# Optimization experiments

Hardware: AMD Instinct MI355X
Metric: run time of the kernel (lower is better)

The kernel has to match this reference:

```python
import jax, jax.numpy as jnp
import numpy as np


def setup_inputs() -> dict:
    key = jax.random.key(0)
    ks = jax.random.split(key, 8)
    B, C, H, W = 4, 512, 64, 64
    M = C // 8
    sq = 1.0 / np.sqrt(C)
    return {
        "x": jax.random.normal(ks[0], (B, C, H, W), jnp.float32),
        "Wq": jax.random.normal(ks[1], (M, C), jnp.float32) * sq,
        "bq": jnp.zeros((M,), jnp.float32),
        "Wk": jax.random.normal(ks[2], (M, C), jnp.float32) * sq,
        "bk": jnp.zeros((M,), jnp.float32),
        "Wv": jax.random.normal(ks[3], (C, C), jnp.float32) * sq,
        "bv": jnp.zeros((C,), jnp.float32),
        "gamma": jax.random.uniform(ks[4], (1,), jnp.float32),
    }


def reference(x, Wq, bq, Wk, bk, Wv, bv, gamma):
    B, C, H, W = x.shape
    N = H * W
    xf = x.reshape(B, C, N)  # flatten spatial -> [B, C, N]
    # 1x1 convs are channel-mixing matmuls
    q = jnp.einsum('mc,bcn->bmn', Wq, xf) + bq[None, :, None]  # [B, M, N]
    k = jnp.einsum('mc,bcn->bmn', Wk, xf) + bk[None, :, None]  # [B, M, N]
    v = jnp.einsum('dc,bcn->bdn', Wv, xf) + bv[None, :, None]  # [B, C, N]
    # sim[b,i,j] = <q[:, i], k[:, j]>, softmax over j
    sim = jnp.einsum('bmi,bmj->bij', q, k)  # [B, N, N]
    attn = jax.nn.softmax(sim, axis=-1)
    # feat[b,c,i] = sum_j v[b,c,j] * attn[b,i,j]
    feat = jnp.einsum('bcj,bij->bci', v, attn)  # [B, C, N]
    out = gamma[0] * feat.reshape(B, C, H, W) + x
    return out
```

## Files before the change

kernel.cpp:

```cpp
#include <hip/hip_runtime.h>

typedef _Float16 f16;
typedef _Float16 f16x8 __attribute__((ext_vector_type(8)));
typedef float    f32x4 __attribute__((ext_vector_type(4)));
typedef unsigned int u32x2 __attribute__((ext_vector_type(2)));

#define B_ 4
#define C_ 512
#define N_ 4096
#define M_ 64

__device__ __forceinline__ unsigned pk2(float a, float b) {
    union { f16 h[2]; unsigned u; } t;
    t.h[0] = (f16)a; t.h[1] = (f16)b;
    return t.u;
}

__global__ __launch_bounds__(256) void transpose_cast(
    const float* __restrict__ x, f16* __restrict__ xtf)
{
    __shared__ float sT[64][65];
    const int n0 = blockIdx.x * 64;
    const int c0 = blockIdx.y * 64;
    const int b  = blockIdx.z;
    const int tid = threadIdx.x;

    #pragma unroll
    for (int i = 0; i < 4; ++i) {
        int e = i * 256 + tid;
        int c = e >> 4;
        int n4 = (e & 15) * 4;
        float4 v = *(const float4*)(x + ((size_t)(b * C_ + c0 + c)) * N_ + n0 + n4);
        sT[c][n4 + 0] = v.x; sT[c][n4 + 1] = v.y;
        sT[c][n4 + 2] = v.z; sT[c][n4 + 3] = v.w;
    }
    __syncthreads();

    const int w = tid >> 6, lane = tid & 63, l15 = lane & 15, quad = lane >> 4;
    #pragma unroll
    for (int j = 0; j < 2; ++j) {
        const int fb  = w * 2 + j;
        const int lnt = fb >> 1, lck = fb & 1;
        const int nl  = lnt * 16 + l15;
        const int cb  = lck * 32 + quad * 8;
        f16x8 o;
        #pragma unroll
        for (int jj = 0; jj < 8; ++jj) o[jj] = (f16)sT[cb + jj][nl];
        const int ntg = (n0 >> 4) + lnt;
        const int ck  = (c0 >> 5) + lck;
        size_t idx = (((size_t)(b * 256 + ntg)) * 16 + ck) * 512 + lane * 8;
        *(f16x8*)(xtf + idx) = o;
    }
}

__global__ __launch_bounds__(512) void qkv_gemm(
    const f16* __restrict__ xtf,
    const float* __restrict__ Wq, const float* __restrict__ bq,
    const float* __restrict__ Wk, const float* __restrict__ bk,
    const float* __restrict__ Wv, const float* __restrict__ bv,
    f16* __restrict__ qt, f16* __restrict__ ktf, f16* __restrict__ vf)
{
    const int tid  = threadIdx.x;
    const int w    = tid >> 6;
    const int lane = tid & 63;
    const int l15  = lane & 15;
    const int quad = lane >> 4;
    const int nBase = blockIdx.x * 128;
    const int oseg  = blockIdx.y;
    const int b     = blockIdx.z;
    const int ot16  = w & 3;
    const int nhalf = w >> 2;

    const float* Wsel;
    if (oseg == 0)      Wsel = Wq;
    else if (oseg == 1) Wsel = Wk;
    else                Wsel = Wv + (size_t)(oseg - 2) * 64 * C_;

    const int orow = ot16 * 16 + l15;
    const float* wp = Wsel + (size_t)orow * C_ + quad * 8;

    const f16* xfb[4];
    #pragma unroll
    for (int ns = 0; ns < 4; ++ns) {
        int ntg = (nBase >> 4) + nhalf * 4 + ns;
        xfb[ns] = xtf + (((size_t)(b * 256 + ntg)) * 16) * 512 + lane * 8;
    }

    f32x4 acc[4] = {};

    float4 w0c = *(const float4*)(wp);
    float4 w1c = *(const float4*)(wp + 4);
    f16x8 b8c[4];
    #pragma unroll
    for (int ns = 0; ns < 4; ++ns) b8c[ns] = *(const f16x8*)(xfb[ns]);

    for (int ck = 0; ck < 16; ++ck) {
        float4 w0n, w1n;
        f16x8  b8n[4];
        if (ck + 1 < 16) {
            w0n = *(const float4*)(wp + ck * 32 + 32);
            w1n = *(const float4*)(wp + ck * 32 + 36);
            #pragma unroll
            for (int ns = 0; ns < 4; ++ns)
                b8n[ns] = *(const f16x8*)(xfb[ns] + (ck + 1) * 512);
        }
        f16x8 a8;
        a8[0]=(f16)w0c.x; a8[1]=(f16)w0c.y; a8[2]=(f16)w0c.z; a8[3]=(f16)w0c.w;
        a8[4]=(f16)w1c.x; a8[5]=(f16)w1c.y; a8[6]=(f16)w1c.z; a8[7]=(f16)w1c.w;
        #pragma unroll
        for (int ns = 0; ns < 4; ++ns)
            acc[ns] = __builtin_amdgcn_mfma_f32_16x16x32_f16(a8, b8c[ns], acc[ns], 0, 0, 0);
        w0c = w0n; w1c = w1n;
        #pragma unroll
        for (int ns = 0; ns < 4; ++ns) b8c[ns] = b8n[ns];
    }

    #pragma unroll
    for (int ns = 0; ns < 4; ++ns) {
        int n = nBase + nhalf * 64 + ns * 16 + l15;
        #pragma unroll
        for (int r = 0; r < 4; ++r) {
            int olocal = ot16 * 16 + quad * 4 + r;
            float bias;
            if (oseg == 0)      bias = bq[olocal];
            else if (oseg == 1) bias = bk[olocal];
            else                bias = bv[(oseg - 2) * 64 + olocal];
            f16 h = (f16)(acc[ns][r] + bias);
            if (oseg == 0) {
                qt[((size_t)(b * N_ + n)) * M_ + olocal] = h;
            } else if (oseg == 1) {
                size_t idx = (((size_t)b * 256 + (n >> 4)) * 2 + (olocal >> 5)) * 512
                           + (size_t)((((olocal >> 3) & 3) * 16 + (n & 15)) * 8) + (olocal & 7);
                ktf[idx] = h;
            } else {
                int c = (oseg - 2) * 64 + olocal;
                size_t idx = ((size_t)b * (C_ * N_)) + (size_t)(c >> 4) * 65536
                           + (size_t)(n >> 6) * 1024 + (size_t)((n >> 5) & 1) * 512
                           + (size_t)((((n >> 3) & 3) * 16 + (c & 15)) * 8) + (n & 7);
                vf[idx] = h;
            }
        }
    }
}

__global__ __launch_bounds__(512, 2) void attn(
    const f16* __restrict__ qt, const f16* __restrict__ ktf,
    const f16* __restrict__ vf, const float* __restrict__ x,
    const float* __restrict__ gamma, float* __restrict__ out)
{
    __shared__ __align__(16) char Pb[2][8192];
    __shared__ float mxs[8][4][16];
    __shared__ float lss[8][4][16];

    const int tid  = threadIdx.x;
    const int w    = tid >> 6;
    const int lane = tid & 63;
    const int l15  = lane & 15;
    const int quad = lane >> 4;
    const int jt   = w & 3;
    const int ish  = w >> 2;
    const int is0  = ish * 2, is1 = is0 + 1;

    const int lin  = blockIdx.x;
    const int b    = (lin & 7) >> 1;
    const int iblk = ((lin >> 3) << 1) | (lin & 1);
    const int i0   = iblk * 64;

    const f16* kln = ktf + (size_t)b * (N_ * M_) + lane * 8;
    const f16* vln = vf  + (size_t)b * (C_ * N_) + lane * 8;

    f16x8 bqf[4][2];
    #pragma unroll
    for (int is = 0; is < 4; ++is)
        #pragma unroll
        for (int kh = 0; kh < 2; ++kh)
            bqf[is][kh] = *(const f16x8*)(qt + ((size_t)(b * N_ + i0 + is * 16 + l15)) * M_
                                          + kh * 32 + quad * 8);

    float mx[4];
    #pragma unroll
    for (int is = 0; is < 4; ++is) mx[is] = -3.0e38f;
    {
        const f16* kw = kln + (size_t)(w * 512) * 64;
        f16x8 akc[4][2];
        #pragma unroll
        for (int t = 0; t < 4; ++t)
            #pragma unroll
            for (int kh = 0; kh < 2; ++kh)
                akc[t][kh] = *(const f16x8*)(kw + t * 1024 + kh * 512);

        #pragma unroll 2
        for (int jj = 0; jj < 512; jj += 64) {
            f16x8 akn[4][2];
            if (jj + 64 < 512) {
                const f16* kn = kw + (size_t)(jj + 64) * 64;
                #pragma unroll
                for (int t = 0; t < 4; ++t)
                    #pragma unroll
                    for (int kh = 0; kh < 2; ++kh)
                        akn[t][kh] = *(const f16x8*)(kn + t * 1024 + kh * 512);
            }
            #pragma unroll
            for (int t = 0; t < 4; ++t) {
                #pragma unroll
                for (int is = 0; is < 4; ++is) {
                    f32x4 s = {};
                    s = __builtin_amdgcn_mfma_f32_16x16x32_f16(akc[t][0], bqf[is][0], s, 0, 0, 0);
                    s = __builtin_amdgcn_mfma_f32_16x16x32_f16(akc[t][1], bqf[is][1], s, 0, 0, 0);
                    mx[is] = fmaxf(mx[is], fmaxf(fmaxf(s[0], s[1]), fmaxf(s[2], s[3])));
                }
            }
            #pragma unroll
            for (int t = 0; t < 4; ++t)
                #pragma unroll
                for (int kh = 0; kh < 2; ++kh)
                    akc[t][kh] = akn[t][kh];
        }
    }
    #pragma unroll
    for (int is = 0; is < 4; ++is) {
        mx[is] = fmaxf(mx[is], __shfl_xor(mx[is], 16, 64));
        mx[is] = fmaxf(mx[is], __shfl_xor(mx[is], 32, 64));
    }
    if (lane < 16) {
        #pragma unroll
        for (int is = 0; is < 4; ++is) mxs[w][is][lane] = mx[is];
    }
    __syncthreads();
    float m0 = -3.0e38f, m1 = -3.0e38f;
    #pragma unroll
    for (int w2 = 0; w2 < 8; ++w2) {
        m0 = fmaxf(m0, mxs[w2][is0][l15]);
        m1 = fmaxf(m1, mxs[w2][is1][l15]);
    }

    f32x4 acc[4][4] = {};
    float lp0 = 0.f, lp1 = 0.f;

    char* pbB = (char*)&Pb[0][0];
    const int swz = (l15 & 7) << 4;
    const int wb0 = ((is0 * 16 + l15) * 128 + (jt * 16 + quad * 4) * 2) ^ swz;
    const int wb1 = wb0 + 2048;
    int rb[4][2];
    #pragma unroll
    for (int is = 0; is < 4; ++is)
        #pragma unroll
        for (int kh = 0; kh < 2; ++kh)
            rb[is][kh] = ((is * 16 + l15) * 128 + kh * 64 + quad * 16) ^ swz;

    const f16* kp = kln + (size_t)(jt * 16) * 64;
    const int cw = w * 4;

    f16x8 ak0 = *(const f16x8*)(kp);
    f16x8 ak1 = *(const f16x8*)(kp + 512);
    {
        f32x4 s0 = {}, s1 = {};
        s0 = __builtin_amdgcn_mfma_f32_16x16x32_f16(ak0, bqf[is0][0], s0, 0, 0, 0);
        s0 = __builtin_amdgcn_mfma_f32_16x16x32_f16(ak1, bqf[is0][1], s0, 0, 0, 0);
        s1 = __builtin_amdgcn_mfma_f32_16x16x32_f16(ak0, bqf[is1][0], s1, 0, 0, 0);
        s1 = __builtin_amdgcn_mfma_f32_16x16x32_f16(ak1, bqf[is1][1], s1, 0, 0, 0);
        float p0 = __expf(s0[0] - m0), p1 = __expf(s0[1] - m0);
        float p2 = __expf(s0[2] - m0), p3 = __expf(s0[3] - m0);
        lp0 += (p0 + p1) + (p2 + p3);
        u32x2 pw0 = { pk2(p0, p1), pk2(p2, p3) };
        *(u32x2*)(pbB + wb0) = pw0;
        float q0 = __expf(s1[0] - m1), q1 = __expf(s1[1] - m1);
        float q2 = __expf(s1[2] - m1), q3 = __expf(s1[3] - m1);
        lp1 += (q0 + q1) + (q2 + q3);
        u32x2 pw1 = { pk2(q0, q1), pk2(q2, q3) };
        *(u32x2*)(pbB + wb1) = pw1;
    }
    ak0 = *(const f16x8*)(kp + 4096);
    ak1 = *(const f16x8*)(kp + 4096 + 512);
    f16x8 vc0[4], vc1[4];
    #pragma unroll
    for (int ct = 0; ct < 4; ++ct) {
        vc0[ct] = *(const f16x8*)(vln + (size_t)(cw + ct) * 65536);
        vc1[ct] = *(const f16x8*)(vln + (size_t)(cw + ct) * 65536 + 512);
    }
    __syncthreads();

    #pragma unroll 2
    for (int t = 0; t < 63; ++t) {
        const int cb = (t & 1) * 8192;
        const int nb = ((t + 1) & 1) * 8192;

        f16x8 pbf[4][2];
        #pragma unroll
        for (int is = 0; is < 4; ++is)
            #pragma unroll
            for (int kh = 0; kh < 2; ++kh)
                pbf[is][kh] = *(const f16x8*)(pbB + cb + rb[is][kh]);

        f32x4 s0 = {}, s1 = {};
        s0 = __builtin_amdgcn_mfma_f32_16x16x32_f16(ak0, bqf[is0][0], s0, 0, 0, 0);
        s0 = __builtin_amdgcn_mfma_f32_16x16x32_f16(ak1, bqf[is0][1], s0, 0, 0, 0);
        s1 = __builtin_amdgcn_mfma_f32_16x16x32_f16(ak0, bqf[is1][0], s1, 0, 0, 0);
        s1 = __builtin_amdgcn_mfma_f32_16x16x32_f16(ak1, bqf[is1][1], s1, 0, 0, 0);

        if (t + 2 < 64) {
            ak0 = *(const f16x8*)(kp + (size_t)(t + 2) * 4096);
            ak1 = *(const f16x8*)(kp + (size_t)(t + 2) * 4096 + 512);
        }
        const f16* vt = vln + (size_t)(t + 1) * 1024;
        f16x8 vn0[4], vn1[4];
        #pragma unroll
        for (int ct = 0; ct < 4; ++ct) {
            vn0[ct] = *(const f16x8*)(vt + (size_t)(cw + ct) * 65536);
            vn1[ct] = *(const f16x8*)(vt + (size_t)(cw + ct) * 65536 + 512);
        }

        {
            float p0 = __expf(s0[0] - m0), p1 = __expf(s0[1] - m0);
            float p2 = __expf(s0[2] - m0), p3 = __expf(s0[3] - m0);
            lp0 += (p0 + p1) + (p2 + p3);
            u32x2 pw = { pk2(p0, p1), pk2(p2, p3) };
            *(u32x2*)(pbB + nb + wb0) = pw;
        }
        {
            float q0 = __expf(s1[0] - m1), q1 = __expf(s1[1] - m1);
            float q2 = __expf(s1[2] - m1), q3 = __expf(s1[3] - m1);
            lp1 += (q0 + q1) + (q2 + q3);
            u32x2 pw = { pk2(q0, q1), pk2(q2, q3) };
            *(u32x2*)(pbB + nb + wb1) = pw;
        }

        __builtin_amdgcn_s_setprio(1);
        #pragma unroll
        for (int ct = 0; ct < 4; ++ct)
            #pragma unroll
            for (int is = 0; is < 4; ++is)
                acc[ct][is] = __builtin_amdgcn_mfma_f32_16x16x32_f16(vc0[ct], pbf[is][0], acc[ct][is], 0, 0, 0);
        #pragma unroll
        for (int ct = 0; ct < 4; ++ct)
            #pragma unroll
            for (int is = 0; is < 4; ++is)
                acc[ct][is] = __builtin_amdgcn_mfma_f32_16x16x32_f16(vc1[ct], pbf[is][1], acc[ct][is], 0, 0, 0);
        __builtin_amdgcn_s_setprio(0);

        __syncthreads();

        #pragma unroll
        for (int ct = 0; ct < 4; ++ct) { vc0[ct] = vn0[ct]; vc1[ct] = vn1[ct]; }
    }

    {
        const int cb = (63 & 1) * 8192;
        f16x8 pbf[4][2];
        #pragma unroll
        for (int is = 0; is < 4; ++is)
            #pragma unroll
            for (int kh = 0; kh < 2; ++kh)
                pbf[is][kh] = *(const f16x8*)(pbB + cb + rb[is][kh]);
        #pragma unroll
        for (int ct = 0; ct < 4; ++ct)
            #pragma unroll
            for (int is = 0; is < 4; ++is)
                acc[ct][is] = __builtin_amdgcn_mfma_f32_16x16x32_f16(vc0[ct], pbf[is][0], acc[ct][is], 0, 0, 0);
        #pragma unroll
        for (int ct = 0; ct < 4; ++ct)
            #pragma unroll
            for (int is = 0; is < 4; ++is)
                acc[ct][is] = __builtin_amdgcn_mfma_f32_16x16x32_f16(vc1[ct], pbf[is][1], acc[ct][is], 0, 0, 0);
    }

    lp0 += __shfl_xor(lp0, 16, 64);
    lp0 += __shfl_xor(lp0, 32, 64);
    lp1 += __shfl_xor(lp1, 16, 64);
    lp1 += __shfl_xor(lp1, 32, 64);
    if (lane < 16) { lss[w][is0][lane] = lp0; lss[w][is1][lane] = lp1; }
    __syncthreads();

    float linv[4];
    #pragma unroll
    for (int is = 0; is < 4; ++is) {
        const int wb = (is >> 1) * 4;
        float l = (lss[wb + 0][is][l15] + lss[wb + 1][is][l15])
                + (lss[wb + 2][is][l15] + lss[wb + 3][is][l15]);
        linv[is] = 1.0f / l;
    }

    const float g = gamma[0];
    #pragma unroll
    for (int is = 0; is < 4; ++is) {
        const int i = i0 + is * 16 + l15;
        #pragma unroll
        for (int ct = 0; ct < 4; ++ct) {
            #pragma unroll
            for (int r = 0; r < 4; ++r) {
                const int c = w * 64 + ct * 16 + quad * 4 + r;
                const size_t idx = ((size_t)(b * C_ + c)) * N_ + i;
                out[idx] = g * (acc[ct][is][r] * linv[is]) + x[idx];
            }
        }
    }
}

extern "C" void kernel_launch(void* const* d_in, const int* in_sizes, int n_in,
                              void* d_out, int out_size, void* d_ws, size_t ws_size,
                              hipStream_t stream)
{
    const float* x     = (const float*)d_in[0];
    const float* Wq    = (const float*)d_in[1];
    const float* bq    = (const float*)d_in[2];
    const float* Wk    = (const float*)d_in[3];
    const float* bk    = (const float*)d_in[4];
    const float* Wv    = (const float*)d_in[5];
    const float* bv    = (const float*)d_in[6];
    const float* gamma = (const float*)d_in[7];
    float* out = (float*)d_out;

    char* ws = (char*)d_ws;
    f16* xtf = (f16*)ws;
    f16* qt  = (f16*)(ws + (size_t)B_ * N_ * C_ * 2);
    f16* ktf = qt + (size_t)B_ * N_ * M_;
    f16* vf  = ktf + (size_t)B_ * N_ * M_;

    transpose_cast<<<dim3(N_ / 64, C_ / 64, B_), 256, 0, stream>>>(x, xtf);
    qkv_gemm<<<dim3(N_ / 128, 10, B_), 512, 0, stream>>>(
        xtf, Wq, bq, Wk, bk, Wv, bv, qt, ktf, vf);
    attn<<<dim3(256), 512, 0, stream>>>(qt, ktf, vf, x, gamma, out);
}
```

Measured before the change: 259.2 us.

## Fuse transpose-cast into QKV GEMM and pre-convert weights to fp16

Removes the separate transpose_cast kernel and its fp16 intermediate copy of x. The QKV projection now reads fp32 x tiles directly into double-buffered shared memory, casts them while building MFMA operands, and computes all 640 output rows per 64-column tile in one block. A small kernel converts the weights to fp16 once per call. Each block now reads x only once instead of ten times across output segments, at the cost of fewer blocks (256), bank-strided LDS column reads, and more accumulator registers.

```diff
diff --git a/kernel.cpp b/kernel.cpp
--- a/kernel.cpp
+++ b/kernel.cpp
@@ -16,128 +16,142 @@
     return t.u;
 }
 
-__global__ __launch_bounds__(256) void transpose_cast(
-    const float* __restrict__ x, f16* __restrict__ xtf)
+__global__ __launch_bounds__(256) void wcvt(
+    const float* __restrict__ Wq, const float* __restrict__ Wk,
+    const float* __restrict__ Wv, f16* __restrict__ Wf)
 {
-    __shared__ float sT[64][65];
-    const int n0 = blockIdx.x * 64;
-    const int c0 = blockIdx.y * 64;
-    const int b  = blockIdx.z;
-    const int tid = threadIdx.x;
-
-    #pragma unroll
-    for (int i = 0; i < 4; ++i) {
-        int e = i * 256 + tid;
-        int c = e >> 4;
-        int n4 = (e & 15) * 4;
-        float4 v = *(const float4*)(x + ((size_t)(b * C_ + c0 + c)) * N_ + n0 + n4);
-        sT[c][n4 + 0] = v.x; sT[c][n4 + 1] = v.y;
-        sT[c][n4 + 2] = v.z; sT[c][n4 + 3] = v.w;
-    }
-    __syncthreads();
-
-    const int w = tid >> 6, lane = tid & 63, l15 = lane & 15, quad = lane >> 4;
-    #pragma unroll
-    for (int j = 0; j < 2; ++j) {
-        const int fb  = w * 2 + j;
-        const int lnt = fb >> 1, lck = fb & 1;
-        const int nl  = lnt * 16 + l15;
-        const int cb  = lck * 32 + quad * 8;
-        f16x8 o;
-        #pragma unroll
-        for (int jj = 0; jj < 8; ++jj) o[jj] = (f16)sT[cb + jj][nl];
-        const int ntg = (n0 >> 4) + lnt;
-        const int ck  = (c0 >> 5) + lck;
-        size_t idx = (((size_t)(b * 256 + ntg)) * 16 + ck) * 512 + lane * 8;
-        *(f16x8*)(xtf + idx) = o;
-    }
+    const int e = (blockIdx.x * 256 + threadIdx.x) * 8;
+    const float* src;
+    int off;
+    if (e < 32768)      { src = Wq; off = e; }
+    else if (e < 65536) { src = Wk; off = e - 32768; }
+    else                { src = Wv; off = e - 65536; }
+    float4 a = *(const float4*)(src + off);
+    float4 b = *(const float4*)(src + off + 4);
+    f16x8 o;
+    o[0]=(f16)a.x; o[1]=(f16)a.y; o[2]=(f16)a.z; o[3]=(f16)a.w;
+    o[4]=(f16)b.x; o[5]=(f16)b.y; o[6]=(f16)b.z; o[7]=(f16)b.w;
+    *(f16x8*)(Wf + e) = o;
 }
 
-__global__ __launch_bounds__(512) void qkv_gemm(
-    const f16* __restrict__ xtf,
-    const float* __restrict__ Wq, const float* __restrict__ bq,
-    const float* __restrict__ Wk, const float* __restrict__ bk,
-    const float* __restrict__ Wv, const float* __restrict__ bv,
+__global__ __launch_bounds__(512) void qkv2(
+    const f16* __restrict__ Wf, const float* __restrict__ x,
+    const float* __restrict__ bq, const float* __restrict__ bk,
+    const float* __restrict__ bv,
     f16* __restrict__ qt, f16* __restrict__ ktf, f16* __restrict__ vf)
 {
+    __shared__ float sX[2][64][65];
+    __shared__ float sBias[640];
+
     const int tid  = threadIdx.x;
     const int w    = tid >> 6;
     const int lane = tid & 63;
     const int l15  = lane & 15;
     const int quad = lane >> 4;
-    const int nBase = blockIdx.x * 128;
-    const int oseg  = blockIdx.y;
-    const int b     = blockIdx.z;
-    const int ot16  = w & 3;
-    const int nhalf = w >> 2;
-
-    const float* Wsel;
-    if (oseg == 0)      Wsel = Wq;
-    else if (oseg == 1) Wsel = Wk;
-    else                Wsel = Wv + (size_t)(oseg - 2) * 64 * C_;
-
-    const int orow = ot16 * 16 + l15;
-    const float* wp = Wsel + (size_t)orow * C_ + quad * 8;
-
-    const f16* xfb[4];
-    #pragma unroll
-    for (int ns = 0; ns < 4; ++ns) {
-        int ntg = (nBase >> 4) + nhalf * 4 + ns;
-        xfb[ns] = xtf + (((size_t)(b * 256 + ntg)) * 16) * 512 + lane * 8;
-    }
-
-    f32x4 acc[4] = {};
-
-    float4 w0c = *(const float4*)(wp);
-    float4 w1c = *(const float4*)(wp + 4);
-    f16x8 b8c[4];
-    #pragma unroll
-    for (int ns = 0; ns < 4; ++ns) b8c[ns] = *(const f16x8*)(xfb[ns]);
-
-    for (int ck = 0; ck < 16; ++ck) {
-        float4 w0n, w1n;
-        f16x8  b8n[4];
-        if (ck + 1 < 16) {
-            w0n = *(const float4*)(wp + ck * 32 + 32);
-            w1n = *(const float4*)(wp + ck * 32 + 36);
-            #pragma unroll
-            for (int ns = 0; ns < 4; ++ns)
-                b8n[ns] = *(const f16x8*)(xfb[ns] + (ck + 1) * 512);
-        }
-        f16x8 a8;
-        a8[0]=(f16)w0c.x; a8[1]=(f16)w0c.y; a8[2]=(f16)w0c.z; a8[3]=(f16)w0c.w;
-        a8[4]=(f16)w1c.x; a8[5]=(f16)w1c.y; a8[6]=(f16)w1c.z; a8[7]=(f16)w1c.w;
-        #pragma unroll
-        for (int ns = 0; ns < 4; ++ns)
-            acc[ns] = __builtin_amdgcn_mfma_f32_16x16x32_f16(a8, b8c[ns], acc[ns], 0, 0, 0);
-        w0c = w0n; w1c = w1n;
-        #pragma unroll
-        for (int ns = 0; ns < 4; ++ns) b8c[ns] = b8n[ns];
-    }
-
-    #pragma unroll
-    for (int ns = 0; ns < 4; ++ns) {
-        int n = nBase + nhalf * 64 + ns * 16 + l15;
-        #pragma unroll
-        for (int r = 0; r < 4; ++r) {
-            int olocal = ot16 * 16 + quad * 4 + r;
-            float bias;
-            if (oseg == 0)      bias = bq[olocal];
-            else if (oseg == 1) bias = bk[olocal];
-            else                bias = bv[(oseg - 2) * 64 + olocal];
-            f16 h = (f16)(acc[ns][r] + bias);
-            if (oseg == 0) {
-                qt[((size_t)(b * N_ + n)) * M_ + olocal] = h;
-            } else if (oseg == 1) {
-                size_t idx = (((size_t)b * 256 + (n >> 4)) * 2 + (olocal >> 5)) * 512
-                           + (size_t)((((olocal >> 3) & 3) * 16 + (n & 15)) * 8) + (olocal & 7);
-                ktf[idx] = h;
+    const int n0   = blockIdx.x * 64;
+    const int b    = blockIdx.y;
+    const int row0 = w * 80;
+
+    for (int e = tid; e < 640; e += 512)
+        sBias[e] = (e < 64) ? bq[e] : (e < 128) ? bk[e - 64] : bv[e - 128];
+
+    {
+        float4 g[2];
+        #pragma unroll
+        for (int i = 0; i < 2; ++i) {
+            int e = i * 512 + tid, c = e >> 4, n4 = (e & 15) * 4;
+            g[i] = *(const float4*)(x + ((size_t)(b * C_ + c)) * N_ + n0 + n4);
+        }
+        #pragma unroll
+        for (int i = 0; i < 2; ++i) {
+            int e = i * 512 + tid, c = e >> 4, n4 = (e & 15) * 4;
+            sX[0][c][n4 + 0] = g[i].x; sX[0][c][n4 + 1] = g[i].y;
+            sX[0][c][n4 + 2] = g[i].z; sX[0][c][n4 + 3] = g[i].w;
+        }
+    }
+
+    f32x4 acc[5][4] = {};
+
+    for (int t = 0; t < 8; ++t) {
+        const int cur = t & 1, nxt = cur ^ 1;
+
+        float4 gn[2];
+        if (t < 7) {
+            #pragma unroll
+            for (int i = 0; i < 2; ++i) {
+                int e = i * 512 + tid, c = e >> 4, n4 = (e & 15) * 4;
+                gn[i] = *(const float4*)(x + ((size_t)(b * C_ + (t + 1) * 64 + c)) * N_ + n0 + n4);
+            }
+        }
+
+        __syncthreads();
+
+        f16x8 af[5][2];
+        #pragma unroll
+        for (int ot = 0; ot < 5; ++ot)
+            #pragma unroll
+            for (int kh = 0; kh < 2; ++kh)
+                af[ot][kh] = *(const f16x8*)(Wf + (size_t)(row0 + ot * 16 + l15) * 512
+                                             + t * 64 + kh * 32 + quad * 8);
+
+        f16x8 bf[4][2];
+        #pragma unroll
+        for (int nt = 0; nt < 4; ++nt)
+            #pragma unroll
+            for (int kh = 0; kh < 2; ++kh) {
+                f16x8 o;
+                #pragma unroll
+                for (int jj = 0; jj < 8; ++jj)
+                    o[jj] = (f16)sX[cur][kh * 32 + quad * 8 + jj][nt * 16 + l15];
+                bf[nt][kh] = o;
+            }
+
+        #pragma unroll
+        for (int ot = 0; ot < 5; ++ot)
+            #pragma unroll
+            for (int kh = 0; kh < 2; ++kh)
+                #pragma unroll
+                for (int nt = 0; nt < 4; ++nt)
+                    acc[ot][nt] = __builtin_amdgcn_mfma_f32_16x16x32_f16(
+                        af[ot][kh], bf[nt][kh], acc[ot][nt], 0, 0, 0);
+
+        if (t < 7) {
+            #pragma unroll
+            for (int i = 0; i < 2; ++i) {
+                int e = i * 512 + tid, c = e >> 4, n4 = (e & 15) * 4;
+                sX[nxt][c][n4 + 0] = gn[i].x; sX[nxt][c][n4 + 1] = gn[i].y;
+                sX[nxt][c][n4 + 2] = gn[i].z; sX[nxt][c][n4 + 3] = gn[i].w;
+            }
+        }
+    }
+
+    #pragma unroll
+    for (int ot = 0; ot < 5; ++ot) {
+        const int rowBase = row0 + ot * 16;
+        const int rq = rowBase + quad * 4;
+        #pragma unroll
+        for (int nt = 0; nt < 4; ++nt) {
+            const int n = n0 + nt * 16 + l15;
+            union { f16 h[4]; unsigned long long u; } pkv;
+            #pragma unroll
+            for (int r = 0; r < 4; ++r)
+                pkv.h[r] = (f16)(acc[ot][nt][r] + sBias[rq + r]);
+            if (rowBase < 64) {
+                *(unsigned long long*)(qt + ((size_t)(b * N_ + n)) * M_ + rq) = pkv.u;
+            } else if (rowBase < 128) {
+                const int ol = rq - 64;
+                size_t idx = (((size_t)b * 256 + (n >> 4)) * 2 + (ol >> 5)) * 512
+                           + (size_t)((((ol >> 3) & 3) * 16 + (n & 15)) * 8) + (ol & 7);
+                *(unsigned long long*)(ktf + idx) = pkv.u;
             } else {
-                int c = (oseg - 2) * 64 + olocal;
-                size_t idx = ((size_t)b * (C_ * N_)) + (size_t)(c >> 4) * 65536
-                           + (size_t)(n >> 6) * 1024 + (size_t)((n >> 5) & 1) * 512
-                           + (size_t)((((n >> 3) & 3) * 16 + (c & 15)) * 8) + (n & 7);
-                vf[idx] = h;
+                const int c = rq - 128;
+                #pragma unroll
+                for (int r = 0; r < 4; ++r) {
+                    size_t idx = ((size_t)b * (C_ * N_)) + (size_t)((c + r) >> 4) * 65536
+                               + (size_t)(n >> 6) * 1024 + (size_t)((n >> 5) & 1) * 512
+                               + (size_t)((((n >> 3) & 3) * 16 + ((c + r) & 15)) * 8) + (n & 7);
+                    vf[idx] = pkv.h[r];
+                }
             }
         }
     }
@@ -411,13 +425,12 @@
     float* out = (float*)d_out;
 
     char* ws = (char*)d_ws;
-    f16* xtf = (f16*)ws;
-    f16* qt  = (f16*)(ws + (size_t)B_ * N_ * C_ * 2);
+    f16* qt  = (f16*)ws;
     f16* ktf = qt + (size_t)B_ * N_ * M_;
     f16* vf  = ktf + (size_t)B_ * N_ * M_;
-
-    transpose_cast<<<dim3(N_ / 64, C_ / 64, B_), 256, 0, stream>>>(x, xtf);
-    qkv_gemm<<<dim3(N_ / 128, 10, B_), 512, 0, stream>>>(
-        xtf, Wq, bq, Wk, bk, Wv, bv, qt, ktf, vf);
+    f16* Wf  = vf + (size_t)B_ * C_ * N_;
+
+    wcvt<<<dim3(160), 256, 0, stream>>>(Wq, Wk, Wv, Wf);
+    qkv2<<<dim3(N_ / 64, B_), 512, 0, stream>>>(Wf, x, bq, bk, bv, qt, ktf, vf);
     attn<<<dim3(256), 512, 0, stream>>>(qt, ktf, vf, x, gamma, out);
 }
```

Result: faster. 224.2 us (-13.5%).
